# Optimization experiments

Hardware: AMD Instinct MI355X
Metric: run time of the kernel (lower is better)

The kernel has to match this reference:

```python
import jax, jax.numpy as jnp
import numpy as np
import math

B, SEQ_LEN, LABEL_LEN, PRED_LEN = 32, 512, 256, 256
D_MODEL, N_HEADS, D_FF = 512, 8, 2048
ENC_IN, DEC_IN, C_OUT, MARK = 21, 21, 21, 4
MA_K, E_LAYERS, D_LAYERS, FACTOR = 25, 2, 1, 1
DEC_LEN = LABEL_LEN + PRED_LEN


def moving_mean(x, k):
    # replicate-pad front/back then avg-pool(kernel=k, stride=1); x: [B,L,C]
    pad = (k - 1) // 2
    xp = jnp.concatenate([jnp.repeat(x[:, :1], pad, axis=1), x,
                          jnp.repeat(x[:, -1:], pad, axis=1)], axis=1)
    cs = jnp.cumsum(xp, axis=1)
    cs = jnp.concatenate([jnp.zeros_like(cs[:, :1]), cs], axis=1)
    return (cs[:, k:] - cs[:, :-k]) / k


def series_decomp(x):
    trend = moving_mean(x, MA_K)
    return x - trend, trend


def circ_conv3(x, W):
    # circular-padded Conv1d kernel=3, no bias; x: [B,L,Cin], W: [3,Cin,Cout]
    xp = jnp.concatenate([x[:, -1:], x, x[:, :1]], axis=1)
    return xp[:, :-2] @ W[0] + xp[:, 1:-1] @ W[1] + xp[:, 2:] @ W[2]


def pos_embed(L, d):
    pos = jnp.arange(L, dtype=jnp.float32)[:, None]
    div = jnp.exp(jnp.arange(0, d, 2, dtype=jnp.float32) * (-math.log(10000.0) / d))
    pe = jnp.zeros((L, d), jnp.float32)
    pe = pe.at[:, 0::2].set(jnp.sin(pos * div)).at[:, 1::2].set(jnp.cos(pos * div))
    return pe


def data_embed(x, x_mark, val_W, time_W):
    # TokenEmbedding (circular conv) + TimeFeatureEmbedding (linear) + PositionalEmbedding
    return circ_conv3(x, val_W) + x_mark @ time_W + pos_embed(x.shape[1], D_MODEL)[None]


def autocorrelation(q, k, v):
    # q: [B,L,H,E]; k,v: [B,S,H,E]  -> [B,L,H,E]
    Bq, L, H, E = q.shape
    S = k.shape[1]
    if L > S:
        pad = jnp.zeros((Bq, L - S, H, E), q.dtype)
        k = jnp.concatenate([k, pad], axis=1)
        v = jnp.concatenate([v, pad], axis=1)
    else:
        k, v = k[:, :L], v[:, :L]
    qf = jnp.fft.rfft(q.transpose(0, 2, 3, 1), axis=-1)
    kf = jnp.fft.rfft(k.transpose(0, 2, 3, 1), axis=-1)
    corr = jnp.fft.irfft(qf * jnp.conj(kf), n=L, axis=-1)   # [B,H,E,L]
    vals = v.transpose(0, 2, 3, 1)                          # [B,H,E,L]
    top_k = int(FACTOR * math.log(L))
    mean_corr = corr.mean(axis=(1, 2))                      # [B,L]
    weights, delay = jax.lax.top_k(mean_corr, top_k)        # [B,K]
    w = jax.nn.softmax(weights, axis=-1)
    # gather from doubled values == circular shift by delay
    idx = (jnp.arange(L)[None, None, :] + delay[:, :, None]) % L   # [B,K,L]
    pat = jnp.take_along_axis(vals[:, None], idx[:, :, None, None, :], axis=-1)  # [B,K,H,E,L]
    agg = jnp.einsum('bkhel,bk->bhel', pat, w)
    return agg.transpose(0, 3, 1, 2)


def ac_layer(qx, kx, vx, Wq, Wk, Wv, Wo):
    Bq, L, D = qx.shape
    dk = D // N_HEADS
    q = (qx @ Wq).reshape(Bq, L, N_HEADS, dk)
    k = (kx @ Wk).reshape(Bq, kx.shape[1], N_HEADS, dk)
    v = (vx @ Wv).reshape(Bq, vx.shape[1], N_HEADS, dk)
    return autocorrelation(q, k, v).reshape(Bq, L, D) @ Wo


def ffn(x, W1, W2):
    # Conv1d kernel=1 (no bias) pair == pointwise MLP
    return jax.nn.gelu(x @ W1, approximate=False) @ W2


def seasonal_ln(x, g, b):
    mu = x.mean(-1, keepdims=True)
    var = ((x - mu) ** 2).mean(-1, keepdims=True)
    xh = (x - mu) / jnp.sqrt(var + 1e-5) * g + b
    return xh - xh.mean(axis=1, keepdims=True)


def encoder_layer(x, Wq, Wk, Wv, Wo, W1, W2):
    x = x + ac_layer(x, x, x, Wq, Wk, Wv, Wo)
    x, _ = series_decomp(x)
    y = ffn(x, W1, W2)
    x, _ = series_decomp(x + y)
    return x


def decoder_layer(x, cross, sWq, sWk, sWv, sWo, cWq, cWk, cWv, cWo, W1, W2, trend_W):
    x = x + ac_layer(x, x, x, sWq, sWk, sWv, sWo)
    x, t1 = series_decomp(x)
    x = x + ac_layer(x, cross, cross, cWq, cWk, cWv, cWo)
    x, t2 = series_decomp(x)
    y = ffn(x, W1, W2)
    x, t3 = series_decomp(x + y)
    residual_trend = circ_conv3(t1 + t2 + t3, trend_W)   # [B,L,C_OUT]
    return x, residual_trend


def _forward(x_enc, x_mark_enc, x_dec, x_mark_dec,
             enc_val_W, enc_time_W, enc_Wq, enc_Wk, enc_Wv, enc_Wo, enc_W1, enc_W2,
             enc_norm_g, enc_norm_b, dec_val_W, dec_time_W,
             dec_sWq, dec_sWk, dec_sWv, dec_sWo, dec_cWq, dec_cWk, dec_cWv, dec_cWo,
             dec_W1, dec_W2, dec_trend_W, dec_norm_g, dec_norm_b, proj_W, proj_b):
    mean = jnp.repeat(x_enc.mean(axis=1, keepdims=True), PRED_LEN, axis=1)
    zeros = jnp.zeros((x_dec.shape[0], PRED_LEN, x_dec.shape[2]), x_enc.dtype)
    seasonal_init, trend_init = series_decomp(x_enc)
    trend_init = jnp.concatenate([trend_init[:, -LABEL_LEN:], mean], axis=1)
    seasonal_init = jnp.concatenate([seasonal_init[:, -LABEL_LEN:], zeros], axis=1)
    enc = data_embed(x_enc, x_mark_enc, enc_val_W, enc_time_W)
    for i in range(E_LAYERS):
        enc = encoder_layer(enc, enc_Wq[i], enc_Wk[i], enc_Wv[i], enc_Wo[i], enc_W1[i], enc_W2[i])
    enc = seasonal_ln(enc, enc_norm_g, enc_norm_b)
    dec = data_embed(seasonal_init, x_mark_dec, dec_val_W, dec_time_W)
    trend = trend_init
    for i in range(D_LAYERS):
        dec, rt = decoder_layer(dec, enc, dec_sWq[i], dec_sWk[i], dec_sWv[i], dec_sWo[i],
                                dec_cWq[i], dec_cWk[i], dec_cWv[i], dec_cWo[i],
                                dec_W1[i], dec_W2[i], dec_trend_W[i])
        trend = trend + rt
    dec = seasonal_ln(dec, dec_norm_g, dec_norm_b)
    dec_out = dec @ proj_W + proj_b + trend
    return dec_out[:, -PRED_LEN:]


def setup_inputs() -> dict:
    key = jax.random.key(0)
    it = iter(jax.random.split(key, 40))
    def rn(shape, s=1.0):
        return jax.random.normal(next(it), shape, jnp.float32) * s
    W = 0.02
    return {
        'x_enc': rn((B, SEQ_LEN, ENC_IN)),
        'x_mark_enc': rn((B, SEQ_LEN, MARK)),
        'x_dec': rn((B, DEC_LEN, DEC_IN)),
        'x_mark_dec': rn((B, DEC_LEN, MARK)),
        'enc_val_W': rn((3, ENC_IN, D_MODEL), W),
        'enc_time_W': rn((MARK, D_MODEL), W),
        'enc_Wq': rn((E_LAYERS, D_MODEL, D_MODEL), W),
        'enc_Wk': rn((E_LAYERS, D_MODEL, D_MODEL), W),
        'enc_Wv': rn((E_LAYERS, D_MODEL, D_MODEL), W),
        'enc_Wo': rn((E_LAYERS, D_MODEL, D_MODEL), W),
        'enc_W1': rn((E_LAYERS, D_MODEL, D_FF), W),
        'enc_W2': rn((E_LAYERS, D_FF, D_MODEL), W),
        'enc_norm_g': jnp.ones((D_MODEL,), jnp.float32),
        'enc_norm_b': jnp.zeros((D_MODEL,), jnp.float32),
        'dec_val_W': rn((3, DEC_IN, D_MODEL), W),
        'dec_time_W': rn((MARK, D_MODEL), W),
        'dec_sWq': rn((D_LAYERS, D_MODEL, D_MODEL), W),
        'dec_sWk': rn((D_LAYERS, D_MODEL, D_MODEL), W),
        'dec_sWv': rn((D_LAYERS, D_MODEL, D_MODEL), W),
        'dec_sWo': rn((D_LAYERS, D_MODEL, D_MODEL), W),
        'dec_cWq': rn((D_LAYERS, D_MODEL, D_MODEL), W),
        'dec_cWk': rn((D_LAYERS, D_MODEL, D_MODEL), W),
        'dec_cWv': rn((D_LAYERS, D_MODEL, D_MODEL), W),
        'dec_cWo': rn((D_LAYERS, D_MODEL, D_MODEL), W),
        'dec_W1': rn((D_LAYERS, D_MODEL, D_FF), W),
        'dec_W2': rn((D_LAYERS, D_FF, D_MODEL), W),
        'dec_trend_W': rn((D_LAYERS, 3, D_MODEL, C_OUT), W),
        'dec_norm_g': jnp.ones((D_MODEL,), jnp.float32),
        'dec_norm_b': jnp.zeros((D_MODEL,), jnp.float32),
        'proj_W': rn((D_MODEL, C_OUT), W),
        'proj_b': jnp.zeros((C_OUT,), jnp.float32),
    }


def reference(x_enc, x_mark_enc, x_dec, x_mark_dec,
              enc_val_W, enc_time_W, enc_Wq, enc_Wk, enc_Wv, enc_Wo, enc_W1, enc_W2,
              enc_norm_g, enc_norm_b, dec_val_W, dec_time_W,
              dec_sWq, dec_sWk, dec_sWv, dec_sWo, dec_cWq, dec_cWk, dec_cWv, dec_cWo,
              dec_W1, dec_W2, dec_trend_W, dec_norm_g, dec_norm_b, proj_W, proj_b):
    return _forward(x_enc, x_mark_enc, x_dec, x_mark_dec,
                    enc_val_W, enc_time_W, enc_Wq, enc_Wk, enc_Wv, enc_Wo, enc_W1, enc_W2,
                    enc_norm_g, enc_norm_b, dec_val_W, dec_time_W,
                    dec_sWq, dec_sWk, dec_sWv, dec_sWo, dec_cWq, dec_cWk, dec_cWv, dec_cWo,
                    dec_W1, dec_W2, dec_trend_W, dec_norm_g, dec_norm_b, proj_W, proj_b)
```

## Files before the change

kernel.cpp:

```cpp
#include <hip/hip_runtime.h>


typedef _Float16 h8 __attribute__((ext_vector_type(8)));
typedef _Float16 h4 __attribute__((ext_vector_type(4)));
typedef float f32x4 __attribute__((ext_vector_type(4)));

struct P12 { const float* p[12]; };
struct P6  { const float* p[6]; };
struct P4  { const float* p[4]; };

__device__ __forceinline__ float gelu_f(float x){
    return 0.5f * x * (1.0f + erff(x * 0.70710678118654752f));
}

__device__ __forceinline__ void gl_lds(const _Float16* gp, _Float16* lp) {
    __builtin_amdgcn_global_load_lds(
        (const __attribute__((address_space(1))) void*)gp,
        (__attribute__((address_space(3))) void*)lp, 16, 0, 0);
}

__global__ void zero_k(float* __restrict__ p, long n){
    long i = (long)blockIdx.x * 256 + threadIdx.x;
    if (i < n) p[i] = 0.f;
}

template<int EPI, int OUT>
__global__ __launch_bounds__(256)
void hgemm_k(const _Float16* __restrict__ A, int lda, int loA,
             const _Float16* __restrict__ Bm, int ldb, int loB,
             const _Float16* __restrict__ Rc, void* __restrict__ Cv,
             int ldc, int loC, int K, int nph, float osc,
             long sA, long sB, long sC)
{
    __shared__ _Float16 As[128 * 64];
    __shared__ _Float16 Bs[128 * 64];
    const int bz = blockIdx.z;
    const int tid = threadIdx.x, lane = tid & 63, w = tid >> 6;
    const int wr = w >> 1, wc = w & 1;
    const _Float16* Ap = A + bz * sA + (long)(blockIdx.y * 128) * lda;
    const _Float16* Bp = Bm + bz * sB + (long)(blockIdx.x * 128) * ldb;

    const int swz = ((lane & 7) ^ ((lane >> 3) & 7)) * 8;
    const int rsub = w * 32 + (lane >> 3);
    const _Float16* ApT = Ap + (long)rsub * lda + swz;
    const _Float16* BpT = Bp + (long)rsub * ldb + swz;
    _Float16* AsT = As + w * 2048;
    _Float16* BsT = Bs + w * 2048;

    const int tpp = K >> 6;
    const int nkt = tpp * nph;
    f32x4 acc[4][4] = {};

    int p = 0, q = 0;
    for (int kt = 0; kt < nkt; ++kt) {
        const int aoff = q * 64 + (p == 2 ? loA : 0);
        const int boff = q * 64 + (p == 1 ? loB : 0);
        __syncthreads();
#pragma unroll
        for (int i = 0; i < 4; i++) {
            gl_lds(ApT + (long)i * 8 * lda + aoff, AsT + i * 512);
            gl_lds(BpT + (long)i * 8 * ldb + boff, BsT + i * 512);
        }
        __syncthreads();
#pragma unroll
        for (int kk = 0; kk < 2; ++kk) {
            h8 af[4], bf[4];
            const int ks = kk * 4 + (lane >> 4);
#pragma unroll
            for (int m = 0; m < 4; m++) {
                int rowa = wr * 64 + m * 16 + (lane & 15);
                af[m] = *(const h8*)(As + rowa * 64 + ((ks ^ (rowa & 7)) * 8));
                int rowb = wc * 64 + m * 16 + (lane & 15);
                bf[m] = *(const h8*)(Bs + rowb * 64 + ((ks ^ (rowb & 7)) * 8));
            }
#pragma unroll
            for (int m = 0; m < 4; m++)
#pragma unroll
                for (int n = 0; n < 4; n++)
                    acc[m][n] = __builtin_amdgcn_mfma_f32_16x16x32_f16(af[m], bf[n], acc[m][n], 0, 0, 0);
        }
        if (++q == tpp) { q = 0; ++p; }
    }

    const int crow0 = blockIdx.y * 128 + wr * 64 + (lane >> 4) * 4;
    const int ccol0 = blockIdx.x * 128 + wc * 64 + (lane & 15);
    if constexpr (OUT == 0) {
        float* Cp = (float*)Cv + (long)bz * sC;
#pragma unroll
        for (int m = 0; m < 4; m++)
#pragma unroll
            for (int n = 0; n < 4; n++) {
                int col = ccol0 + n * 16;
#pragma unroll
                for (int r2 = 0; r2 < 4; r2++) {
                    long idx = (long)(crow0 + m * 16 + r2) * ldc + col;
                    Cp[idx] = acc[m][n][r2] * osc;
                }
            }
    } else if constexpr (OUT == 1) {
        _Float16* Cp = (_Float16*)Cv + (long)bz * sC;
#pragma unroll
        for (int m = 0; m < 4; m++)
#pragma unroll
            for (int n = 0; n < 4; n++) {
                int col = ccol0 + n * 16;
#pragma unroll
                for (int r2 = 0; r2 < 4; r2++) {
                    int row = crow0 + m * 16 + r2;
                    long base = (long)row * ldc + col;
                    float v = acc[m][n][r2] * osc;
                    if (EPI == 1) {
                        long rb = (long)row * 1024 + col;
                        v += (float)Rc[rb] + (float)Rc[rb + 512];
                    }
                    if (EPI == 2) v = gelu_f(v);
                    _Float16 hi = (_Float16)v;
                    Cp[base] = hi;
                    if (loC >= 0) Cp[base + loC] = (_Float16)(v - (float)hi);
                }
            }
    } else {
        __shared__ float diag[512];
        float* mc = (float*)Cv + (long)bz * sC;
        for (int t = tid; t < 512; t += 256) diag[t] = 0.f;
        __syncthreads();
#pragma unroll
        for (int m = 0; m < 4; m++)
#pragma unroll
            for (int n = 0; n < 4; n++) {
                int col = ccol0 + n * 16;
#pragma unroll
                for (int r2 = 0; r2 < 4; r2++) {
                    int row = crow0 + m * 16 + r2;
                    atomicAdd(&diag[(row - col) & 511], acc[m][n][r2]);
                }
            }
        __syncthreads();
        for (int t = tid; t < 512; t += 256) {
            float v = diag[t];
            if (v != 0.f) atomicAdd(&mc[t], v);
        }
    }
}

__global__ __launch_bounds__(256)
void hgemmAgg_k(const _Float16* __restrict__ KV,
                const int* __restrict__ delays, const float* __restrict__ wts,
                const _Float16* __restrict__ Bm,
                const _Float16* __restrict__ Rc, _Float16* __restrict__ Cp,
                float osc)
{
    __shared__ _Float16 As[128 * 64];
    __shared__ _Float16 Bs[128 * 64];
    const int tid = threadIdx.x, lane = tid & 63, w = tid >> 6;
    const int wr = w >> 1, wc = w & 1;
    const _Float16* Bp = Bm + (long)(blockIdx.x * 128) * 1024;

    const int swz = ((lane & 7) ^ ((lane >> 3) & 7)) * 8;
    const int rsub = w * 32 + (lane >> 3);
    const _Float16* BpT = Bp + (long)rsub * 1024 + swz;
    _Float16* BsT = Bs + w * 2048;

    const int rowblk = blockIdx.y * 128;
    const int b = (rowblk + rsub) >> 9;
    int dl[6]; float wv[6];
#pragma unroll
    for (int k = 0; k < 6; k++) { dl[k] = delays[b * 6 + k]; wv[k] = wts[b * 6 + k]; }
    const _Float16* KVb = KV + ((long)b << 19);

    f32x4 acc[4][4] = {};
    for (int q = 0; q < 8; ++q) {
        const int coff = q * 64 + swz;
        __syncthreads();
#pragma unroll
        for (int i = 0; i < 4; i++) {
            int l = (rowblk + rsub + i * 8) & 511;
            float s8[8] = {};
#pragma unroll
            for (int k = 0; k < 6; k++) {
                const h8 v = *(const h8*)(KVb + ((long)((l + dl[k]) & 511) << 10) + coff);
#pragma unroll
                for (int j = 0; j < 8; j++) s8[j] = fmaf(wv[k], (float)v[j], s8[j]);
            }
            h8 hv;
#pragma unroll
            for (int j = 0; j < 8; j++) hv[j] = (_Float16)s8[j];
            *(h8*)(As + w * 2048 + i * 512 + lane * 8) = hv;
            gl_lds(BpT + (long)i * 8 * 1024 + q * 64, BsT + i * 512);
        }
        __syncthreads();
#pragma unroll
        for (int kk = 0; kk < 2; ++kk) {
            h8 af[4], bf[4];
            const int ks = kk * 4 + (lane >> 4);
#pragma unroll
            for (int m = 0; m < 4; m++) {
                int rowa = wr * 64 + m * 16 + (lane & 15);
                af[m] = *(const h8*)(As + rowa * 64 + ((ks ^ (rowa & 7)) * 8));
                int rowb = wc * 64 + m * 16 + (lane & 15);
                bf[m] = *(const h8*)(Bs + rowb * 64 + ((ks ^ (rowb & 7)) * 8));
            }
#pragma unroll
            for (int m = 0; m < 4; m++)
#pragma unroll
                for (int n = 0; n < 4; n++)
                    acc[m][n] = __builtin_amdgcn_mfma_f32_16x16x32_f16(af[m], bf[n], acc[m][n], 0, 0, 0);
        }
    }

    const int crow0 = rowblk + wr * 64 + (lane >> 4) * 4;
    const int ccol0 = blockIdx.x * 128 + wc * 64 + (lane & 15);
#pragma unroll
    for (int m = 0; m < 4; m++)
#pragma unroll
        for (int n = 0; n < 4; n++) {
            int col = ccol0 + n * 16;
#pragma unroll
            for (int r2 = 0; r2 < 4; r2++) {
                int row = crow0 + m * 16 + r2;
                long rb = (long)row * 1024 + col;
                float v = acc[m][n][r2] * osc + (float)Rc[rb] + (float)Rc[rb + 512];
                _Float16 hi = (_Float16)v;
                Cp[rb] = hi;
                Cp[rb + 512] = (_Float16)(v - (float)hi);
            }
        }
}

__global__ __launch_bounds__(256)
void splitAll_k(P12 ps, _Float16* __restrict__ PA, _Float16* __restrict__ PB)
{
    const int m = blockIdx.y;
    const float* __restrict__ src = ps.p[m];
    _Float16* dst;
    if (m < 4)      dst = PA + (long)(2 * m) * 524288;
    else if (m < 8) dst = PB + (long)(2 * (m - 4)) * 524288;
    else            dst = PB + (long)(2 * (m - 8) + 1) * 524288;
    long t = (long)blockIdx.x * 256 + threadIdx.x;
    long row = t >> 6; int kc = (int)(t & 63) * 8;
    const float4 v0 = *(const float4*)(src + row * 512 + kc);
    const float4 v1 = *(const float4*)(src + row * 512 + kc + 4);
    float vv[8] = {v0.x,v0.y,v0.z,v0.w,v1.x,v1.y,v1.z,v1.w};
    h8 hi, lo;
#pragma unroll
    for (int j = 0; j < 8; j++) {
        float s = vv[j] * 64.f;
        _Float16 h = (_Float16)s;
        hi[j] = h; lo[j] = (_Float16)(s - (float)h);
    }
    *(h8*)(dst + row * 1024 + kc)       = hi;
    *(h8*)(dst + row * 1024 + 512 + kc) = lo;
}

__global__ __launch_bounds__(256)
void convWoAll_k(P4 ps, _Float16* __restrict__ PA)
{
    const int z = blockIdx.z;
    const float* __restrict__ src = ps.p[z];
    _Float16* dst = PA + (long)(2 * z + 1) * 524288;
    __shared__ float t[32][33];
    int k0 = blockIdx.x * 32, n0 = blockIdx.y * 32, tid = threadIdx.x;
#pragma unroll
    for (int i = 0; i < 4; i++) {
        int lin = tid + i * 256; int r = lin >> 5, c = lin & 31;
        t[r][c] = src[(long)(k0 + r) * 512 + n0 + c];
    }
    __syncthreads();
#pragma unroll
    for (int i = 0; i < 4; i++) {
        int lin = tid + i * 256; int n = lin >> 5, k = lin & 31;
        float v = t[k][n] * 64.f;
        _Float16 hi = (_Float16)v;
        long base = (long)(n0 + n) * 1024 + k0 + k;
        dst[base]       = hi;
        dst[base + 512] = (_Float16)(v - (float)hi);
    }
}

__global__ __launch_bounds__(256)
void convW2All_k(P6 ps, _Float16* __restrict__ encW1C, _Float16* __restrict__ encW2C,
                 _Float16* __restrict__ dW1C, _Float16* __restrict__ dW2C)
{
    const int z = blockIdx.z;
    const float* __restrict__ src = ps.p[z];
    _Float16* dst = (z==0) ? encW1C : (z==1) ? encW1C + 2097152 : (z==2) ? dW1C :
                    (z==3) ? encW2C : (z==4) ? encW2C + 2097152 : dW2C;
    const bool isW1 = z < 3;
    const int N = isW1 ? 2048 : 512;
    const int K = isW1 ? 512 : 2048;
    int k0 = (isW1 ? blockIdx.x : blockIdx.y) * 32;
    int n0 = (isW1 ? blockIdx.y : blockIdx.x) * 32;
    __shared__ float t[32][33];
    int tid = threadIdx.x;
#pragma unroll
    for (int i = 0; i < 4; i++) {
        int lin = tid + i * 256; int r = lin >> 5, c = lin & 31;
        t[r][c] = src[(long)(k0 + r) * N + n0 + c];
    }
    __syncthreads();
#pragma unroll
    for (int i = 0; i < 4; i++) {
        int lin = tid + i * 256; int n = lin >> 5, k = lin & 31;
        float v = t[k][n];
        _Float16 hi = (_Float16)v;
        long base = (long)(n0 + n) * 2 * K + k0 + k;
        dst[base]     = hi;
        dst[base + K] = (_Float16)(v - (float)hi);
    }
}

__global__ void convW63_k(const float* __restrict__ W, _Float16* __restrict__ dst)
{
    int i = blockIdx.x * 256 + threadIdx.x;
    int k = i & 511, j = i >> 9;
    float v = (j < 63) ? 64.f * W[(long)(j / 21) * 10752 + (long)k * 21 + (j % 21)] : 0.f;
    _Float16 hi = (_Float16)v;
    dst[(long)j * 1024 + k]       = hi;
    dst[(long)j * 1024 + 512 + k] = (_Float16)(v - (float)hi);
}

__global__ __launch_bounds__(256)
void embed_k(const float* __restrict__ x, const float* __restrict__ mark,
             const float* __restrict__ valW, const float* __restrict__ timeW,
             _Float16* __restrict__ cat)
{
    const int lg = blockIdx.x, dh = blockIdx.y, b = blockIdx.z;
    const int tid = threadIdx.x;
    const int dd = dh * 256 + tid;
    const int l0 = lg * 8;
    __shared__ float xs[10][21];
    __shared__ float mk[8][4];
    if (tid < 210) {
        int r = tid / 21, c = tid % 21;
        int ll = (l0 - 1 + r + 512) & 511;
        xs[r][c] = x[((long)b * 512 + ll) * 21 + c];
    }
    if (tid >= 224 && tid < 256) {
        int t2 = tid - 224, il = t2 >> 2, m = t2 & 3;
        mk[il][m] = mark[((long)b * 512 + l0 + il) * 4 + m];
    }
    __syncthreads();
    float acc[8];
#pragma unroll
    for (int il = 0; il < 8; il++) acc[il] = 0.f;
    for (int t = 0; t < 3; t++)
        for (int c = 0; c < 21; c++) {
            float w = valW[(t * 21 + c) * 512 + dd];
#pragma unroll
            for (int il = 0; il < 8; il++)
                acc[il] = fmaf(xs[il + t][c], w, acc[il]);
        }
    for (int m = 0; m < 4; m++) {
        float w = timeW[m * 512 + dd];
#pragma unroll
        for (int il = 0; il < 8; il++)
            acc[il] = fmaf(mk[il][m], w, acc[il]);
    }
    const float freq = expf((float)(dd & ~1) * (-9.210340371976184f / 512.0f));
#pragma unroll
    for (int il = 0; il < 8; il++) {
        float ang = (float)(l0 + il) * freq;
        float pe = (dd & 1) ? cosf(ang) : sinf(ang);
        float v = acc[il] + pe;
        long row = (long)b * 512 + l0 + il;
        _Float16 hi = (_Float16)v;
        cat[row * 1024 + dd]       = hi;
        cat[row * 1024 + 512 + dd] = (_Float16)(v - (float)hi);
    }
}

template<int TREND>
__global__ __launch_bounds__(256)
void decompW_k(const _Float16* __restrict__ xc, _Float16* __restrict__ outc,
               _Float16* __restrict__ tsc)
{
    long t = (long)blockIdx.x * 256 + threadIdx.x;
    long rowg = t >> 7; int d4 = (int)(t & 127) * 4;
    int lg = (int)(rowg & 63); long b = rowg >> 6;
    const int l0 = lg * 8;
    const _Float16* xb = xc + (b << 19);
    float s[8][4] = {};
    float xo[8][4];
#pragma unroll
    for (int rr = -12; rr <= 19; rr++) {
        int rc = l0 + rr; rc = rc < 0 ? 0 : (rc > 511 ? 511 : rc);
        h4 vh = *(const h4*)(xb + ((long)rc << 10) + d4);
        h4 vl = *(const h4*)(xb + ((long)rc << 10) + 512 + d4);
        float vv[4];
#pragma unroll
        for (int j = 0; j < 4; j++) vv[j] = (float)vh[j] + (float)vl[j];
#pragma unroll
        for (int i = 0; i < 8; i++) {
            if (i >= rr - 12 && i <= rr + 12) {
#pragma unroll
                for (int j = 0; j < 4; j++) s[i][j] += vv[j];
            }
        }
        if (rr >= 0 && rr < 8) {
#pragma unroll
            for (int j = 0; j < 4; j++) xo[rr][j] = vv[j];
        }
    }
#pragma unroll
    for (int i = 0; i < 8; i++) {
        long row = b * 512 + l0 + i;
        float tr[4], ov[4];
#pragma unroll
        for (int j = 0; j < 4; j++) {
            tr[j] = s[i][j] * (1.f / 25.f);
            ov[j] = xo[i][j] - tr[j];
        }
        h4 hi, lo;
#pragma unroll
        for (int j = 0; j < 4; j++) {
            _Float16 h = (_Float16)ov[j];
            hi[j] = h; lo[j] = (_Float16)(ov[j] - (float)h);
        }
        *(h4*)(outc + row * 1024 + d4)       = hi;
        *(h4*)(outc + row * 1024 + 512 + d4) = lo;
        if (TREND) {
            _Float16* tp = tsc + row * 1024 + d4;
            if (TREND == 1) {
                h4 th = *(h4*)tp, tl = *(h4*)(tp + 512);
#pragma unroll
                for (int j = 0; j < 4; j++) tr[j] += (float)th[j] + (float)tl[j];
            }
            h4 th2, tl2;
#pragma unroll
            for (int j = 0; j < 4; j++) {
                _Float16 h = (_Float16)tr[j];
                th2[j] = h; tl2[j] = (_Float16)(tr[j] - (float)h);
            }
            *(h4*)tp         = th2;
            *(h4*)(tp + 512) = tl2;
        }
    }
}

__global__ __launch_bounds__(512)
void meanseq2_k(const float* __restrict__ x, float* __restrict__ xm)
{
    int b = blockIdx.x, tid = threadIdx.x;
    __shared__ float sd[504];
    if (tid < 504) {
        int c = tid % 21, g = tid / 21;
        int l0 = g * 22, l1 = l0 + 22 > 512 ? 512 : l0 + 22;
        const float* xb = x + (long)b * 10752;
        float s = 0.f;
        for (int l = l0; l < l1; l++) s += xb[l * 21 + c];
        sd[tid] = s;
    }
    __syncthreads();
    if (tid < 21) {
        float t = 0.f;
#pragma unroll
        for (int g = 0; g < 24; g++) t += sd[g * 21 + tid];
        xm[b * 21 + tid] = t * (1.f / 512.f);
    }
}

__global__ void prep_k(const float* __restrict__ x, const float* __restrict__ xm,
                       float* __restrict__ sinit, float* __restrict__ tinit, int total)
{
    int i = blockIdx.x * 256 + threadIdx.x;
    if (i >= total) return;
    int c = i % 21, l = (i / 21) % 512, b = i / 10752;
    if (l < 256) {
        int lc = 256 + l;
        float s = 0.f;
        for (int j = -12; j <= 12; j++) {
            int ll = lc + j; ll = ll > 511 ? 511 : ll;
            s += x[((long)b * 512 + ll) * 21 + c];
        }
        float t = s * (1.f / 25.f);
        tinit[i] = t;
        sinit[i] = x[((long)b * 512 + lc) * 21 + c] - t;
    } else {
        sinit[i] = 0.f;
        tinit[i] = xm[b * 21 + c];
    }
}

__global__ __launch_bounds__(256)
void topk_k(float* __restrict__ mc, int* __restrict__ delays,
            float* __restrict__ wts)
{
    const float SCL = 1.f / (512.f * 4096.f);
    int b = blockIdx.x, tid = threadIdx.x;
    __shared__ float v[512];
    __shared__ float rv[256];
    __shared__ int   ri[256];
    __shared__ float selv[6];
    v[tid]       = mc[b * 512 + tid]       * SCL;
    v[tid + 256] = mc[b * 512 + tid + 256] * SCL;
    mc[b * 512 + tid] = 0.f;
    mc[b * 512 + tid + 256] = 0.f;
    __syncthreads();
    for (int p = 0; p < 6; p++) {
        float bv = v[tid]; int bi = tid;
        float v2 = v[tid + 256];
        if (v2 > bv) { bv = v2; bi = tid + 256; }
        rv[tid] = bv; ri[tid] = bi;
        __syncthreads();
        for (int s = 128; s > 0; s >>= 1) {
            if (tid < s) {
                float ov = rv[tid + s]; int oi = ri[tid + s];
                if (ov > rv[tid] || (ov == rv[tid] && oi < ri[tid])) {
                    rv[tid] = ov; ri[tid] = oi;
                }
            }
            __syncthreads();
        }
        if (tid == 0) { selv[p] = rv[0]; delays[b * 6 + p] = ri[0]; v[ri[0]] = -3.4e38f; }
        __syncthreads();
    }
    if (tid == 0) {
        float mx = selv[0];
        for (int p = 1; p < 6; p++) mx = fmaxf(mx, selv[p]);
        float e[6], sum = 0.f;
        for (int p = 0; p < 6; p++) { e[p] = expf(selv[p] - mx); sum += e[p]; }
        for (int p = 0; p < 6; p++) wts[b * 6 + p] = e[p] / sum;
    }
}

__global__ __launch_bounds__(256)
void ln_k(const _Float16* __restrict__ xc, const float* __restrict__ g,
          const float* __restrict__ be, float* __restrict__ out)
{
    int row = blockIdx.x, tid = threadIdx.x;
    const _Float16* xr = xc + ((long)row << 10);
    float v0 = (float)xr[tid]       + (float)xr[tid + 512];
    float v1 = (float)xr[tid + 256] + (float)xr[tid + 768];
    __shared__ float rs[256];
    rs[tid] = v0 + v1; __syncthreads();
    for (int s = 128; s > 0; s >>= 1) { if (tid < s) rs[tid] += rs[tid + s]; __syncthreads(); }
    float mu = rs[0] * (1.f / 512.f);
    __syncthreads();
    float d0 = v0 - mu, d1 = v1 - mu;
    rs[tid] = d0 * d0 + d1 * d1; __syncthreads();
    for (int s = 128; s > 0; s >>= 1) { if (tid < s) rs[tid] += rs[tid + s]; __syncthreads(); }
    float rstd = 1.0f / sqrtf(rs[0] * (1.f / 512.f) + 1e-5f);
    out[((long)row << 9) + tid]       = d0 * rstd * g[tid] + be[tid];
    out[((long)row << 9) + tid + 256] = d1 * rstd * g[tid + 256] + be[tid + 256];
}

__global__ __launch_bounds__(256)
void colsum_k(const float* __restrict__ x, float* __restrict__ cs)
{
    int d = blockIdx.x * 256 + threadIdx.x;
    int b = blockIdx.y;
    const float* xb = x + ((long)b << 18);
    float s = 0.f;
    for (int l = 0; l < 512; l++) s += xb[((long)l << 9) + d];
    cs[((long)b << 9) + d] = s;
}

__global__ __launch_bounds__(256)
void subcolcat_k(const float* __restrict__ x, const float* __restrict__ cs,
                 _Float16* __restrict__ cat)
{
    long t = (long)blockIdx.x * 256 + threadIdx.x;
    long row = t >> 6; int d8 = (int)(t & 63) * 8;
    int b = (int)(row >> 9);
    const float4* c4 = (const float4*)(cs + ((long)b << 9) + d8);
    float4 m0 = c4[0], m1 = c4[1];
    float m[8] = {m0.x,m0.y,m0.z,m0.w,m1.x,m1.y,m1.z,m1.w};
    const float4* xp = (const float4*)(x + row * 512 + d8);
    float4 x0 = xp[0], x1 = xp[1];
    float v[8] = {x0.x,x0.y,x0.z,x0.w,x1.x,x1.y,x1.z,x1.w};
    h8 hi, lo;
#pragma unroll
    for (int j = 0; j < 8; j++) {
        float vv = v[j] - m[j] * (1.f / 512.f);
        _Float16 h = (_Float16)vv;
        hi[j] = h; lo[j] = (_Float16)(vv - (float)h);
    }
    *(h8*)(cat + row * 1024 + d8)       = hi;
    *(h8*)(cat + row * 1024 + 512 + d8) = lo;
}

__global__ void proj_k(const float* __restrict__ x, const float* __restrict__ cs,
                       const float* __restrict__ pw, const float* __restrict__ pb,
                       const float* __restrict__ tinit, const float* __restrict__ H,
                       float* __restrict__ out, int total)
{
    int i = blockIdx.x * 256 + threadIdx.x;
    if (i >= total) return;
    int c = i % 21, l = (i / 21) % 256 + 256, b = i / 5376;
    const float* xr = x + ((long)(b * 512 + l) << 9);
    const float* csb = cs + ((long)b << 9);
    float s = 0.f;
    for (int d = 0; d < 512; d++)
        s = fmaf(xr[d] - csb[d] * (1.f / 512.f), pw[d * 21 + c], s);
    long r = (long)b * 512;
    float trend = tinit[b * 10752 + l * 21 + c]
                + H[(r + ((l + 511) & 511)) * 128 + c]
                + H[(r + l) * 128 + 21 + c]
                + H[(r + ((l + 1) & 511)) * 128 + 42 + c];
    out[i] = s + pb[c] + trend;
}

static void hgemm(int mode, int nph, float osc,
                  const _Float16* A, int lda, int loA,
                  const _Float16* B, int ldb, int loB,
                  const _Float16* Rc, void* C, int ldc, int loC,
                  int K, int M, int N, int batch,
                  long sA, long sB, long sC, hipStream_t st)
{
    dim3 g(N / 128, M / 128, batch), blk(256);
    switch (mode) {
    case 0:  hgemm_k<0,1><<<g,blk,0,st>>>(A,lda,loA,B,ldb,loB,Rc,C,ldc,loC,K,nph,osc,sA,sB,sC); break;
    case 2:  hgemm_k<2,1><<<g,blk,0,st>>>(A,lda,loA,B,ldb,loB,Rc,C,ldc,loC,K,nph,osc,sA,sB,sC); break;
    case 12: hgemm_k<1,1><<<g,blk,0,st>>>(A,lda,loA,B,ldb,loB,Rc,C,ldc,loC,K,nph,osc,sA,sB,sC); break;
    case 11: hgemm_k<0,0><<<g,blk,0,st>>>(A,lda,loA,B,ldb,loB,Rc,C,ldc,loC,K,nph,osc,sA,sB,sC); break;
    default: hgemm_k<0,2><<<g,blk,0,st>>>(A,lda,loA,B,ldb,loB,Rc,C,ldc,loC,K,nph,osc,sA,sB,sC); break;
    }
}

extern "C" void kernel_launch(void* const* d_in, const int* in_sizes, int n_in,
                              void* d_out, int out_size, void* d_ws, size_t ws_size,
                              hipStream_t stream)
{
    const float* x_enc    = (const float*)d_in[0];
    const float* xm_enc   = (const float*)d_in[1];
    const float* xm_dec   = (const float*)d_in[3];
    const float* enc_valW = (const float*)d_in[4];
    const float* enc_timeW= (const float*)d_in[5];
    const float* enc_Wq   = (const float*)d_in[6];
    const float* enc_Wk   = (const float*)d_in[7];
    const float* enc_Wv   = (const float*)d_in[8];
    const float* enc_Wo   = (const float*)d_in[9];
    const float* enc_W1   = (const float*)d_in[10];
    const float* enc_W2   = (const float*)d_in[11];
    const float* enc_g    = (const float*)d_in[12];
    const float* enc_b    = (const float*)d_in[13];
    const float* dec_valW = (const float*)d_in[14];
    const float* dec_timeW= (const float*)d_in[15];
    const float* sWq = (const float*)d_in[16];
    const float* sWk = (const float*)d_in[17];
    const float* sWv = (const float*)d_in[18];
    const float* sWo = (const float*)d_in[19];
    const float* cWq = (const float*)d_in[20];
    const float* cWk = (const float*)d_in[21];
    const float* cWv = (const float*)d_in[22];
    const float* cWo = (const float*)d_in[23];
    const float* dW1 = (const float*)d_in[24];
    const float* dW2 = (const float*)d_in[25];
    const float* dtW = (const float*)d_in[26];
    const float* dec_g = (const float*)d_in[27];
    const float* dec_b = (const float*)d_in[28];
    const float* projW = (const float*)d_in[29];
    const float* projB = (const float*)d_in[30];

    const size_t W_BYTES = 50000000;
    const size_t perB = 8000000;
    int Bc = 32;
    while (Bc > 1 && W_BYTES + (size_t)Bc * perB + (4u << 20) > ws_size) Bc >>= 1;

    char* wp = (char*)d_ws;
    auto alloc = [&](size_t bytes) { char* p = wp; wp += (bytes + 255) & ~(size_t)255; return p; };

    _Float16* Wcat8  = (_Float16*)alloc(8 * 524288 * 2);
    _Float16* encW1C = (_Float16*)alloc(2 * 2097152 * 2);
    _Float16* encW2C = (_Float16*)alloc(2 * 2097152 * 2);
    _Float16* dW1C   = (_Float16*)alloc(2097152 * 2);
    _Float16* dW2C   = (_Float16*)alloc(2097152 * 2);
    _Float16* W63C   = (_Float16*)alloc(131072 * 2);
    _Float16* PA     = (_Float16*)alloc(8 * 524288 * 2);
    _Float16* PB     = (_Float16*)alloc(8 * 524288 * 2);

    const long ROWS = (long)Bc * 512;
    _Float16* cX     = (_Float16*)alloc(ROWS * 1024 * 2);
    _Float16* cO     = (_Float16*)alloc(ROWS * 1024 * 2);
    _Float16* TSc    = (_Float16*)alloc(ROWS * 1024 * 2);
    _Float16* ENCcat = (_Float16*)alloc(ROWS * 1024 * 2);
    _Float16* bigcat = (_Float16*)alloc(ROWS * 2048 * 2);
    float* F       = (float*)alloc(ROWS * 512 * 4);
    float* H       = (float*)alloc(ROWS * 128 * 4);
    float* sinit   = (float*)alloc((long)Bc * 10752 * 4);
    float* tinit   = (float*)alloc((long)Bc * 10752 * 4);
    float* xmean   = (float*)alloc((long)Bc * 21 * 4);
    float* mc      = (float*)alloc((long)Bc * 512 * 4);
    float* cs      = (float*)alloc((long)Bc * 512 * 4);
    float* wts     = (float*)alloc((long)Bc * 6 * 4);
    int*   delays  = (int*)alloc((long)Bc * 6 * 4);

    dim3 cb(256);
    P12 sp;
    sp.p[0] = enc_Wk;  sp.p[1] = enc_Wk + 262144;
    sp.p[2] = sWk;     sp.p[3] = cWk;
    sp.p[4] = enc_Wq;  sp.p[5] = enc_Wq + 262144;
    sp.p[6] = sWq;     sp.p[7] = cWq;
    sp.p[8] = enc_Wv;  sp.p[9] = enc_Wv + 262144;
    sp.p[10] = sWv;    sp.p[11] = cWv;
    P4 op;
    op.p[0] = enc_Wo;  op.p[1] = enc_Wo + 262144;
    op.p[2] = sWo;     op.p[3] = cWo;
    P6 fp;
    fp.p[0] = enc_W1;  fp.p[1] = enc_W1 + 1048576; fp.p[2] = dW1;
    fp.p[3] = enc_W2;  fp.p[4] = enc_W2 + 1048576; fp.p[5] = dW2;
    splitAll_k <<<dim3(128,12), cb, 0, stream>>>(sp, PA, PB);
    convWoAll_k<<<dim3(16,16,4), cb, 0, stream>>>(op, PA);
    hgemm(0, 3, 1.f, PA,1024,512, PB,1024,512, nullptr, Wcat8, 1024, 512,
          512, 512, 512, 8, 524288, 524288, 524288, stream);
    convW2All_k<<<dim3(16,64,6), cb, 0, stream>>>(fp, encW1C, encW2C, dW1C, dW2C);
    convW63_k  <<<256, cb, 0, stream>>>(dtW, W63C);

    const int M = (int)ROWS;
    const int t21 = Bc * 10752;
    const int gRows = Bc * 128;
    const int gW = Bc * 32;
    const long sCA = 512 * 1024;
    const float IOS = 1.f / 4096.f;

    zero_k<<<(Bc*512 + 255)/256, 256, 0, stream>>>(mc, Bc*512);

    auto attn = [&](const _Float16* cIn, _Float16* cOut,
                    const _Float16* KVcat, int slot) {
        const _Float16* WqkC_ = Wcat8 + (long)(2*slot)     * 524288;
        const _Float16* WvoC_ = Wcat8 + (long)(2*slot + 1) * 524288;
        hgemm(0, 3, 1.f, cIn,1024,512, WqkC_,1024,512, nullptr, bigcat, 1024, 512,
              512, M, 512, 1, 0,0,0, stream);
        hgemm(20, 3, 1.f, bigcat,1024,512, KVcat,1024,512, nullptr, mc, 0, 0,
              512, 512, 512, Bc, sCA, sCA, 512, stream);
        topk_k<<<Bc, 256, 0, stream>>>(mc, delays, wts);
        hgemmAgg_k<<<dim3(4, M/128), 256, 0, stream>>>(KVcat, delays, wts,
                                                       WvoC_, cIn, cOut, IOS);
    };
    auto ffn = [&](const _Float16* cIn, _Float16* cOut,
                   const _Float16* W1C, const _Float16* W2C) {
        hgemm(2, 1, 1.f, cIn,1024,512, W1C,1024,512, nullptr, bigcat, 2048, -1,
              512, M, 2048, 1, 0,0,0, stream);
        hgemm(12, 1, 1.f, bigcat,2048,0, W2C,4096,2048, cIn, cOut, 1024, 512,
              2048, M, 512, 1, 0,0,0, stream);
    };

    for (int b0 = 0; b0 < 32; b0 += Bc) {
        const float* xe  = x_enc  + (long)b0 * 10752;
        const float* mke = xm_enc + (long)b0 * 2048;
        const float* mkd = xm_dec + (long)b0 * 2048;
        float* outp = (float*)d_out + (long)b0 * 5376;

        meanseq2_k<<<Bc, 512, 0, stream>>>(xe, xmean);
        prep_k    <<<(t21 + 255)/256, 256, 0, stream>>>(xe, xmean, sinit, tinit, t21);

        embed_k<<<dim3(64,2,Bc), 256, 0, stream>>>(xe, mke, enc_valW, enc_timeW, cX);
        for (int L = 0; L < 2; L++) {
            attn(cX, cO, cX, L);
            decompW_k<0><<<gW, 256, 0, stream>>>(cO, cX, nullptr);
            ffn(cX, cO, encW1C + (long)L*2097152, encW2C + (long)L*2097152);
            decompW_k<0><<<gW, 256, 0, stream>>>(cO, cX, nullptr);
        }
        ln_k       <<<Bc*512, 256, 0, stream>>>(cX, enc_g, enc_b, F);
        colsum_k   <<<dim3(2,Bc), 256, 0, stream>>>(F, cs);
        subcolcat_k<<<gRows, 256, 0, stream>>>(F, cs, ENCcat);

        embed_k<<<dim3(64,2,Bc), 256, 0, stream>>>(sinit, mkd, dec_valW, dec_timeW, cX);

        attn(cX, cO, cX, 2);
        decompW_k<2><<<gW, 256, 0, stream>>>(cO, cX, TSc);
        attn(cX, cO, ENCcat, 3);
        decompW_k<1><<<gW, 256, 0, stream>>>(cO, cX, TSc);
        ffn(cX, cO, dW1C, dW2C);
        decompW_k<1><<<gW, 256, 0, stream>>>(cO, cX, TSc);

        hgemm(11, 1, 1.f/64.f, TSc,1024,512, W63C,1024,512, nullptr, H, 128, 0,
              512, M, 128, 1, 0,0,0, stream);
        ln_k    <<<Bc*512, 256, 0, stream>>>(cX, dec_g, dec_b, F);
        colsum_k<<<dim3(2,Bc), 256, 0, stream>>>(F, cs);
        proj_k  <<<(Bc*5376+255)/256, 256, 0, stream>>>(F, cs, projW, projB,
                                                        tinit, H, outp, Bc*5376);
    }
}
```

Before: 2.230 ms.

## Fuse top-k into aggregation GEMM, fold mc zeroing, split column sums

The separate topk_k launch is removed. Each hgemmAgg_k block now recomputes the per-batch top-6 delays and softmax weights from the correlation sums in shared memory before its GEMM, so every block repeats that small reduction. Zeroing of the correlation accumulator moves into meanseq2_k and decompW_k, which removes the standalone zero kernel. The column-sum kernel is split into 8 chunked partials to expose more parallelism, and subcolcat_k and proj_k now add the partials themselves.

```diff
diff --git a/kernel.cpp b/kernel.cpp
--- a/kernel.cpp
+++ b/kernel.cpp
@@ -17,11 +17,6 @@
     __builtin_amdgcn_global_load_lds(
         (const __attribute__((address_space(1))) void*)gp,
         (__attribute__((address_space(3))) void*)lp, 16, 0, 0);
-}
-
-__global__ void zero_k(float* __restrict__ p, long n){
-    long i = (long)blockIdx.x * 256 + threadIdx.x;
-    if (i < n) p[i] = 0.f;
 }
 
 template<int EPI, int OUT>
@@ -144,8 +139,7 @@
 }
 
 __global__ __launch_bounds__(256)
-void hgemmAgg_k(const _Float16* __restrict__ KV,
-                const int* __restrict__ delays, const float* __restrict__ wts,
+void hgemmAgg_k(const _Float16* __restrict__ KV, const float* __restrict__ mc,
                 const _Float16* __restrict__ Bm,
                 const _Float16* __restrict__ Rc, _Float16* __restrict__ Cp,
                 float osc)
@@ -154,18 +148,51 @@
     __shared__ _Float16 Bs[128 * 64];
     const int tid = threadIdx.x, lane = tid & 63, w = tid >> 6;
     const int wr = w >> 1, wc = w & 1;
+    const int rowblk = blockIdx.y * 128;
+    const int b = rowblk >> 9;
+
+    int dl[6]; float wv[6];
+    {
+        float* v  = (float*)As;
+        float* rv = (float*)As + 512;
+        int*   ri = (int*)Bs;
+        const float SCL = 1.f / (512.f * 4096.f);
+        v[tid]       = mc[b * 512 + tid]       * SCL;
+        v[tid + 256] = mc[b * 512 + tid + 256] * SCL;
+        __syncthreads();
+        float sv[6];
+        for (int p = 0; p < 6; p++) {
+            float bv = v[tid]; int bi = tid;
+            float v2 = v[tid + 256];
+            if (v2 > bv) { bv = v2; bi = tid + 256; }
+            rv[tid] = bv; ri[tid] = bi;
+            __syncthreads();
+            for (int s = 128; s > 0; s >>= 1) {
+                if (tid < s) {
+                    float ov = rv[tid + s]; int oi = ri[tid + s];
+                    if (ov > rv[tid] || (ov == rv[tid] && oi < ri[tid])) {
+                        rv[tid] = ov; ri[tid] = oi;
+                    }
+                }
+                __syncthreads();
+            }
+            sv[p] = rv[0]; dl[p] = ri[0];
+            __syncthreads();
+            if (tid == 0) v[ri[0]] = -3.4e38f;
+            __syncthreads();
+        }
+        float mx = sv[0];
+        for (int p = 1; p < 6; p++) mx = fmaxf(mx, sv[p]);
+        float e[6], sum = 0.f;
+        for (int p = 0; p < 6; p++) { e[p] = expf(sv[p] - mx); sum += e[p]; }
+        for (int p = 0; p < 6; p++) wv[p] = e[p] / sum;
+    }
+
     const _Float16* Bp = Bm + (long)(blockIdx.x * 128) * 1024;
-
     const int swz = ((lane & 7) ^ ((lane >> 3) & 7)) * 8;
     const int rsub = w * 32 + (lane >> 3);
     const _Float16* BpT = Bp + (long)rsub * 1024 + swz;
     _Float16* BsT = Bs + w * 2048;
-
-    const int rowblk = blockIdx.y * 128;
-    const int b = (rowblk + rsub) >> 9;
-    int dl[6]; float wv[6];
-#pragma unroll
-    for (int k = 0; k < 6; k++) { dl[k] = delays[b * 6 + k]; wv[k] = wts[b * 6 + k]; }
     const _Float16* KVb = KV + ((long)b << 19);
 
     f32x4 acc[4][4] = {};
@@ -372,9 +399,10 @@
 template<int TREND>
 __global__ __launch_bounds__(256)
 void decompW_k(const _Float16* __restrict__ xc, _Float16* __restrict__ outc,
-               _Float16* __restrict__ tsc)
+               _Float16* __restrict__ tsc, float* __restrict__ mcz, int nMc)
 {
     long t = (long)blockIdx.x * 256 + threadIdx.x;
+    if (t < nMc) mcz[t] = 0.f;
     long rowg = t >> 7; int d4 = (int)(t & 127) * 4;
     int lg = (int)(rowg & 63); long b = rowg >> 6;
     const int l0 = lg * 8;
@@ -438,9 +466,11 @@
 }
 
 __global__ __launch_bounds__(512)
-void meanseq2_k(const float* __restrict__ x, float* __restrict__ xm)
+void meanseq2_k(const float* __restrict__ x, float* __restrict__ xm,
+                float* __restrict__ mcz)
 {
     int b = blockIdx.x, tid = threadIdx.x;
+    mcz[b * 512 + tid] = 0.f;
     __shared__ float sd[504];
     if (tid < 504) {
         int c = tid % 21, g = tid / 21;
@@ -478,48 +508,6 @@
     } else {
         sinit[i] = 0.f;
         tinit[i] = xm[b * 21 + c];
-    }
-}
-
-__global__ __launch_bounds__(256)
-void topk_k(float* __restrict__ mc, int* __restrict__ delays,
-            float* __restrict__ wts)
-{
-    const float SCL = 1.f / (512.f * 4096.f);
-    int b = blockIdx.x, tid = threadIdx.x;
-    __shared__ float v[512];
-    __shared__ float rv[256];
-    __shared__ int   ri[256];
-    __shared__ float selv[6];
-    v[tid]       = mc[b * 512 + tid]       * SCL;
-    v[tid + 256] = mc[b * 512 + tid + 256] * SCL;
-    mc[b * 512 + tid] = 0.f;
-    mc[b * 512 + tid + 256] = 0.f;
-    __syncthreads();
-    for (int p = 0; p < 6; p++) {
-        float bv = v[tid]; int bi = tid;
-        float v2 = v[tid + 256];
-        if (v2 > bv) { bv = v2; bi = tid + 256; }
-        rv[tid] = bv; ri[tid] = bi;
-        __syncthreads();
-        for (int s = 128; s > 0; s >>= 1) {
-            if (tid < s) {
-                float ov = rv[tid + s]; int oi = ri[tid + s];
-                if (ov > rv[tid] || (ov == rv[tid] && oi < ri[tid])) {
-                    rv[tid] = ov; ri[tid] = oi;
-                }
-            }
-            __syncthreads();
-        }
-        if (tid == 0) { selv[p] = rv[0]; delays[b * 6 + p] = ri[0]; v[ri[0]] = -3.4e38f; }
-        __syncthreads();
-    }
-    if (tid == 0) {
-        float mx = selv[0];
-        for (int p = 1; p < 6; p++) mx = fmaxf(mx, selv[p]);
-        float e[6], sum = 0.f;
-        for (int p = 0; p < 6; p++) { e[p] = expf(selv[p] - mx); sum += e[p]; }
-        for (int p = 0; p < 6; p++) wts[b * 6 + p] = e[p] / sum;
     }
 }
 
@@ -544,27 +532,31 @@
     out[((long)row << 9) + tid + 256] = d1 * rstd * g[tid + 256] + be[tid + 256];
 }
 
-__global__ __launch_bounds__(256)
-void colsum_k(const float* __restrict__ x, float* __restrict__ cs)
+__global__ void colpart_k(const float* __restrict__ x, float* __restrict__ cp)
 {
     int d = blockIdx.x * 256 + threadIdx.x;
-    int b = blockIdx.y;
+    int ch = blockIdx.y, b = blockIdx.z;
     const float* xb = x + ((long)b << 18);
     float s = 0.f;
-    for (int l = 0; l < 512; l++) s += xb[((long)l << 9) + d];
-    cs[((long)b << 9) + d] = s;
-}
-
-__global__ __launch_bounds__(256)
-void subcolcat_k(const float* __restrict__ x, const float* __restrict__ cs,
+    for (int l = ch * 64; l < ch * 64 + 64; l++) s += xb[((long)l << 9) + d];
+    cp[((long)(b * 8 + ch) << 9) + d] = s;
+}
+
+__global__ __launch_bounds__(256)
+void subcolcat_k(const float* __restrict__ x, const float* __restrict__ cp,
                  _Float16* __restrict__ cat)
 {
     long t = (long)blockIdx.x * 256 + threadIdx.x;
     long row = t >> 6; int d8 = (int)(t & 63) * 8;
     int b = (int)(row >> 9);
-    const float4* c4 = (const float4*)(cs + ((long)b << 9) + d8);
-    float4 m0 = c4[0], m1 = c4[1];
-    float m[8] = {m0.x,m0.y,m0.z,m0.w,m1.x,m1.y,m1.z,m1.w};
+    float m[8] = {};
+#pragma unroll
+    for (int ch = 0; ch < 8; ch++) {
+        const float4* c4 = (const float4*)(cp + ((long)(b * 8 + ch) << 9) + d8);
+        float4 c0 = c4[0], c1 = c4[1];
+        m[0]+=c0.x; m[1]+=c0.y; m[2]+=c0.z; m[3]+=c0.w;
+        m[4]+=c1.x; m[5]+=c1.y; m[6]+=c1.z; m[7]+=c1.w;
+    }
     const float4* xp = (const float4*)(x + row * 512 + d8);
     float4 x0 = xp[0], x1 = xp[1];
     float v[8] = {x0.x,x0.y,x0.z,x0.w,x1.x,x1.y,x1.z,x1.w};
@@ -579,7 +571,7 @@
     *(h8*)(cat + row * 1024 + 512 + d8) = lo;
 }
 
-__global__ void proj_k(const float* __restrict__ x, const float* __restrict__ cs,
+__global__ void proj_k(const float* __restrict__ x, const float* __restrict__ cp,
                        const float* __restrict__ pw, const float* __restrict__ pb,
                        const float* __restrict__ tinit, const float* __restrict__ H,
                        float* __restrict__ out, int total)
@@ -588,10 +580,13 @@
     if (i >= total) return;
     int c = i % 21, l = (i / 21) % 256 + 256, b = i / 5376;
     const float* xr = x + ((long)(b * 512 + l) << 9);
-    const float* csb = cs + ((long)b << 9);
     float s = 0.f;
-    for (int d = 0; d < 512; d++)
-        s = fmaf(xr[d] - csb[d] * (1.f / 512.f), pw[d * 21 + c], s);
+    for (int d = 0; d < 512; d++) {
+        float m = 0.f;
+#pragma unroll
+        for (int ch = 0; ch < 8; ch++) m += cp[((long)(b * 8 + ch) << 9) + d];
+        s = fmaf(xr[d] - m * (1.f / 512.f), pw[d * 21 + c], s);
+    }
     long r = (long)b * 512;
     float trend = tinit[b * 10752 + l * 21 + c]
                 + H[(r + ((l + 511) & 511)) * 128 + c]
@@ -681,9 +676,7 @@
     float* tinit   = (float*)alloc((long)Bc * 10752 * 4);
     float* xmean   = (float*)alloc((long)Bc * 21 * 4);
     float* mc      = (float*)alloc((long)Bc * 512 * 4);
-    float* cs      = (float*)alloc((long)Bc * 512 * 4);
-    float* wts     = (float*)alloc((long)Bc * 6 * 4);
-    int*   delays  = (int*)alloc((long)Bc * 6 * 4);
+    float* cp      = (float*)alloc((long)Bc * 4096 * 4);
 
     dim3 cb(256);
     P12 sp;
@@ -710,10 +703,9 @@
     const int t21 = Bc * 10752;
     const int gRows = Bc * 128;
     const int gW = Bc * 32;
+    const int nMc = Bc * 512;
     const long sCA = 512 * 1024;
     const float IOS = 1.f / 4096.f;
-
-    zero_k<<<(Bc*512 + 255)/256, 256, 0, stream>>>(mc, Bc*512);
 
     auto attn = [&](const _Float16* cIn, _Float16* cOut,
                     const _Float16* KVcat, int slot) {
@@ -723,9 +715,7 @@
               512, M, 512, 1, 0,0,0, stream);
         hgemm(20, 3, 1.f, bigcat,1024,512, KVcat,1024,512, nullptr, mc, 0, 0,
               512, 512, 512, Bc, sCA, sCA, 512, stream);
-        topk_k<<<Bc, 256, 0, stream>>>(mc, delays, wts);
-        hgemmAgg_k<<<dim3(4, M/128), 256, 0, stream>>>(KVcat, delays, wts,
-                                                       WvoC_, cIn, cOut, IOS);
+        hgemmAgg_k<<<dim3(4, M/128), 256, 0, stream>>>(KVcat, mc, WvoC_, cIn, cOut, IOS);
     };
     auto ffn = [&](const _Float16* cIn, _Float16* cOut,
                    const _Float16* W1C, const _Float16* W2C) {
@@ -741,34 +731,34 @@
         const float* mkd = xm_dec + (long)b0 * 2048;
         float* outp = (float*)d_out + (long)b0 * 5376;
 
-        meanseq2_k<<<Bc, 512, 0, stream>>>(xe, xmean);
+        meanseq2_k<<<Bc, 512, 0, stream>>>(xe, xmean, mc);
         prep_k    <<<(t21 + 255)/256, 256, 0, stream>>>(xe, xmean, sinit, tinit, t21);
 
         embed_k<<<dim3(64,2,Bc), 256, 0, stream>>>(xe, mke, enc_valW, enc_timeW, cX);
         for (int L = 0; L < 2; L++) {
             attn(cX, cO, cX, L);
-            decompW_k<0><<<gW, 256, 0, stream>>>(cO, cX, nullptr);
+            decompW_k<0><<<gW, 256, 0, stream>>>(cO, cX, nullptr, mc, nMc);
             ffn(cX, cO, encW1C + (long)L*2097152, encW2C + (long)L*2097152);
-            decompW_k<0><<<gW, 256, 0, stream>>>(cO, cX, nullptr);
+            decompW_k<0><<<gW, 256, 0, stream>>>(cO, cX, nullptr, mc, nMc);
         }
         ln_k       <<<Bc*512, 256, 0, stream>>>(cX, enc_g, enc_b, F);
-        colsum_k   <<<dim3(2,Bc), 256, 0, stream>>>(F, cs);
-        subcolcat_k<<<gRows, 256, 0, stream>>>(F, cs, ENCcat);
+        colpart_k  <<<dim3(2,8,Bc), 256, 0, stream>>>(F, cp);
+        subcolcat_k<<<gRows, 256, 0, stream>>>(F, cp, ENCcat);
 
         embed_k<<<dim3(64,2,Bc), 256, 0, stream>>>(sinit, mkd, dec_valW, dec_timeW, cX);
 
         attn(cX, cO, cX, 2);
-        decompW_k<2><<<gW, 256, 0, stream>>>(cO, cX, TSc);
+        decompW_k<2><<<gW, 256, 0, stream>>>(cO, cX, TSc, mc, nMc);
         attn(cX, cO, ENCcat, 3);
-        decompW_k<1><<<gW, 256, 0, stream>>>(cO, cX, TSc);
+        decompW_k<1><<<gW, 256, 0, stream>>>(cO, cX, TSc, mc, nMc);
         ffn(cX, cO, dW1C, dW2C);
-        decompW_k<1><<<gW, 256, 0, stream>>>(cO, cX, TSc);
+        decompW_k<1><<<gW, 256, 0, stream>>>(cO, cX, TSc, mc, nMc);
 
         hgemm(11, 1, 1.f/64.f, TSc,1024,512, W63C,1024,512, nullptr, H, 128, 0,
               512, M, 128, 1, 0,0,0, stream);
-        ln_k    <<<Bc*512, 256, 0, stream>>>(cX, dec_g, dec_b, F);
-        colsum_k<<<dim3(2,Bc), 256, 0, stream>>>(F, cs);
-        proj_k  <<<(Bc*5376+255)/256, 256, 0, stream>>>(F, cs, projW, projB,
-                                                        tinit, H, outp, Bc*5376);
-    }
-}
+        ln_k     <<<Bc*512, 256, 0, stream>>>(cX, dec_g, dec_b, F);
+        colpart_k<<<dim3(2,8,Bc), 256, 0, stream>>>(F, cp);
+        proj_k   <<<(Bc*5376+255)/256, 256, 0, stream>>>(F, cp, projW, projB,
+                                                         tinit, H, outp, Bc*5376);
+    }
+}
```

Result: slower. 2.381 ms (+6.7%).
